# Optimization experiments

Hardware: AMD Instinct MI355X
Metric: run time of the kernel (lower is better)

## Reference

```python
import jax, jax.numpy as jnp
import numpy as np

N = 100000   # n_nodes
E = 1600000  # n_edges
BN_EPS = 1e-5


def setup_inputs() -> dict:
    key = jax.random.key(0)
    ks = jax.random.split(key, 10)
    x = jax.random.normal(ks[0], (N, 20), dtype=jnp.float32)
    edge_index = jax.random.randint(ks[1], (2, E), 0, N, dtype=jnp.int64)
    dims = [(20, 64), (64, 48), (48, 32)]
    inp = {"x": x, "edge_index": edge_index}
    for i, (di, do) in enumerate(dims):
        inp[f"W{i+1}"] = jax.random.normal(ks[2 + i], (di, do), dtype=jnp.float32) / np.sqrt(di)
        inp[f"b{i+1}"] = jnp.zeros((do,), dtype=jnp.float32)
        inp[f"g{i+1}"] = jnp.ones((do,), dtype=jnp.float32)
        inp[f"beta{i+1}"] = jnp.zeros((do,), dtype=jnp.float32)
    return inp


def _gcn_norm(edge_index):
    # add self loops, compute symmetric normalization D^-1/2 (A+I) D^-1/2
    loop = jnp.arange(N, dtype=edge_index.dtype)
    src = jnp.concatenate([edge_index[0], loop])
    dst = jnp.concatenate([edge_index[1], loop])
    deg = jax.ops.segment_sum(jnp.ones_like(src, dtype=jnp.float32), dst, num_segments=N)
    dinv = jax.lax.rsqrt(deg)  # deg >= 1 thanks to self loops
    norm = dinv[src] * dinv[dst]  # [E+N]
    return src, dst, norm


def _gcn_layer(h, src, dst, norm, W, b):
    m = h @ W                                  # [N, out]
    agg = jax.ops.segment_sum(m[src] * norm[:, None], dst, num_segments=N)
    return agg + b


def _batchnorm(x, g, beta):
    mu = jnp.mean(x, axis=0)
    var = jnp.mean(jnp.square(x - mu), axis=0)  # biased, as torch BN training
    return (x - mu) * jax.lax.rsqrt(var + BN_EPS) * g + beta


def reference(x, edge_index, W1, b1, g1, beta1, W2, b2, g2, beta2, W3, b3, g3, beta3):
    src, dst, norm = _gcn_norm(edge_index)
    h = _gcn_layer(x, src, dst, norm, W1, b1)
    h = jax.nn.relu(_batchnorm(h, g1, beta1))   # dropout rate 0 -> identity
    h = _gcn_layer(h, src, dst, norm, W2, b2)
    h = jax.nn.relu(_batchnorm(h, g2, beta2))
    h = _gcn_layer(h, src, dst, norm, W3, b3)
    h = _batchnorm(h, g3, beta3)                # last activation is Identity
    return h
```

## Files before the change

kernel.cpp:

```cpp
#include <hip/hip_runtime.h>


#define NN 100000
#define NE 1600000
constexpr float BN_EPS_F = 1e-5f;

#define BSZ 128
#define NBKT ((NN + BSZ - 1) / BSZ)
#define EC 16384
#define NEB ((NE + EC - 1) / EC)
#define MTOT (NBKT * NEB)
#define CAP 4096


__device__ __forceinline__ unsigned f2bf(float f) {
  union { float f; unsigned u; } v; v.f = f;
  return (v.u + 0x7fffu + ((v.u >> 16) & 1u)) >> 16;
}
__device__ __forceinline__ unsigned pack_bf2(float f0, float f1) {
  return f2bf(f0) | (f2bf(f1) << 16);
}
__device__ __forceinline__ float bf_lo(unsigned u) {
  union { unsigned u; float f; } v; v.u = u << 16; return v.f;
}
__device__ __forceinline__ float bf_hi(unsigned u) {
  union { unsigned u; float f; } v; v.u = u & 0xffff0000u; return v.f;
}


__global__ void hist_pass(const int* __restrict__ dst, int* __restrict__ ph, int e) {
  __shared__ int h[NBKT];
  int tid = threadIdx.x;
  for (int i = tid; i < NBKT; i += 256) h[i] = 0;
  __syncthreads();
  int tbase = blockIdx.x * EC + tid * 64;
#pragma unroll 4
  for (int k = 0; k < 64; k += 4) {
    int i = tbase + k;
    if (i < e) {
      int4 d = *(const int4*)(dst + i);
      atomicAdd(&h[d.x >> 7], 1);
      atomicAdd(&h[d.y >> 7], 1);
      atomicAdd(&h[d.z >> 7], 1);
      atomicAdd(&h[d.w >> 7], 1);
    }
  }
  __syncthreads();
  for (int i = tid; i < NBKT; i += 256) ph[i * NEB + blockIdx.x] = h[i];
}

__global__ void scan_block_sums(const int* __restrict__ data, int* __restrict__ bsums, int n) {
  __shared__ int sd[256];
  int tid = threadIdx.x;
  int base = blockIdx.x * 1024;
  int s = 0;
#pragma unroll
  for (int j = 0; j < 4; j++) {
    int idx = base + tid * 4 + j;
    if (idx < n) s += data[idx];
  }
  sd[tid] = s;
  __syncthreads();
  for (int o = 128; o > 0; o >>= 1) {
    if (tid < o) sd[tid] += sd[tid + o];
    __syncthreads();
  }
  if (tid == 0) bsums[blockIdx.x] = sd[0];
}

__global__ void scan_bsums2(int* __restrict__ bsums, int nb) {
  __shared__ int sd[128];
  int tid = threadIdx.x;
  int v = (tid < nb) ? bsums[tid] : 0;
  sd[tid] = v;
  __syncthreads();
  for (int o = 1; o < 128; o <<= 1) {
    int t = (tid >= o) ? sd[tid - o] : 0;
    __syncthreads();
    sd[tid] += t;
    __syncthreads();
  }
  if (tid < nb) bsums[tid] = sd[tid] - v;
}

__global__ void scan_apply(int* __restrict__ data, const int* __restrict__ bsums, int n) {
  __shared__ int sd[256];
  int tid = threadIdx.x;
  int base = blockIdx.x * 1024;
  int c[4];
  int s = 0;
#pragma unroll
  for (int j = 0; j < 4; j++) {
    int idx = base + tid * 4 + j;
    c[j] = (idx < n) ? data[idx] : 0;
    s += c[j];
  }
  sd[tid] = s;
  __syncthreads();
  for (int o = 1; o < 256; o <<= 1) {
    int t = (tid >= o) ? sd[tid - o] : 0;
    __syncthreads();
    sd[tid] += t;
    __syncthreads();
  }
  int off = bsums[blockIdx.x] + sd[tid] - s;
#pragma unroll
  for (int j = 0; j < 4; j++) {
    int idx = base + tid * 4 + j;
    if (idx < n) {
      data[idx] = off;
      off += c[j];
    }
  }
}

__global__ void bin_pass(const int* __restrict__ src, const int* __restrict__ dst,
                         const int* __restrict__ ph, int* __restrict__ packed, int e) {
  __shared__ int cur[NBKT];
  int tid = threadIdx.x;
  for (int i = tid; i < NBKT; i += 256) cur[i] = ph[i * NEB + blockIdx.x];
  __syncthreads();
  int tbase = blockIdx.x * EC + tid * 64;
#pragma unroll 4
  for (int k = 0; k < 64; k += 4) {
    int i = tbase + k;
    if (i < e) {
      int4 s = *(const int4*)(src + i);
      int4 d = *(const int4*)(dst + i);
      int p0 = atomicAdd(&cur[d.x >> 7], 1);
      int p1 = atomicAdd(&cur[d.y >> 7], 1);
      int p2 = atomicAdd(&cur[d.z >> 7], 1);
      int p3 = atomicAdd(&cur[d.w >> 7], 1);
      packed[p0] = (s.x << 7) | (d.x & 127);
      packed[p1] = (s.y << 7) | (d.y & 127);
      packed[p2] = (s.z << 7) | (d.z & 127);
      packed[p3] = (s.w << 7) | (d.w & 127);
    }
  }
}

__global__ void bucket_finalize(const int* __restrict__ ph, const int* __restrict__ packed,
                                const float* __restrict__ x, int* __restrict__ rowptr,
                                float* __restrict__ dinv, int* __restrict__ csr_src,
                                unsigned* __restrict__ xb) {
  __shared__ int eidx[CAP];
  __shared__ int csr_l[CAP];
  __shared__ int ldeg[BSZ], lscan[BSZ], lcur[BSZ];
  __shared__ float ldinv[BSZ];
  int b = blockIdx.x, tid = threadIdx.x;
  int start = ph[b * NEB];
  int end = (b == NBKT - 1) ? NE : ph[(b + 1) * NEB];
  int cnt = end - start;
  if (cnt > CAP) cnt = CAP;
  for (int i = tid; i < cnt; i += 256) eidx[i] = packed[start + i];
  if (tid < BSZ) ldeg[tid] = 0;
  __syncthreads();
  for (int i = tid; i < cnt; i += 256) atomicAdd(&ldeg[eidx[i] & 127], 1);
  __syncthreads();
  if (tid < BSZ) lscan[tid] = ldeg[tid];
  __syncthreads();
  for (int o = 1; o < BSZ; o <<= 1) {
    int t = 0;
    if (tid < BSZ && tid >= o) t = lscan[tid - o];
    __syncthreads();
    if (tid < BSZ) lscan[tid] += t;
    __syncthreads();
  }
  int gn = b * BSZ + tid;
  if (tid < BSZ) {
    int ex = lscan[tid] - ldeg[tid];
    lcur[tid] = ex;
    float dv = rsqrtf((float)(ldeg[tid] + 1));
    ldinv[tid] = dv;
    if (gn < NN) {
      rowptr[gn] = start + ex;
      dinv[gn] = dv;
    }
  }
  if (b == NBKT - 1 && tid == 0) rowptr[NN] = NE;
  __syncthreads();
  for (int i = tid; i < cnt; i += 256) {
    int pe = eidx[i];
    int pos = atomicAdd(&lcur[pe & 127], 1);
    csr_l[pos] = pe >> 7;
  }
  __syncthreads();
  for (int i = tid; i < cnt; i += 256) csr_src[start + i] = csr_l[i];
  for (int i = tid; i < BSZ * 16; i += 256) {
    int nl = i >> 4, j = i & 15;
    int g2 = b * BSZ + nl;
    if (g2 < NN) {
      unsigned u = 0;
      if (j < 10) {
        float2 f = *(const float2*)(x + (size_t)g2 * 20 + 2 * j);
        float dd = ldinv[nl];
        u = pack_bf2(dd * f.x, dd * f.y);
      }
      xb[(size_t)g2 * 16 + j] = u;
    }
  }
}


__launch_bounds__(256)
__global__ void aggregate_x(const unsigned* __restrict__ mb, const int* __restrict__ rowptr,
                            const int* __restrict__ csr_src, const float* __restrict__ dinv,
                            unsigned* __restrict__ out) {
  int tid = threadIdx.x;
  int sub = tid >> 4, lane = tid & 15;
  int cl = (lane < 10) ? lane : lane - 10;
  int d = blockIdx.x * 16 + sub;
  int start = rowptr[d], end = rowptr[d + 1];
  unsigned su = mb[(size_t)d * 16 + cl];
  float acc0 = bf_lo(su), acc1 = bf_hi(su);
  int j = start;
  int aligned = (start + 3) & ~3;
  int pe = aligned < end ? aligned : end;
  for (; j < pe; j++) {
    unsigned u = mb[(size_t)csr_src[j] * 16 + cl];
    acc0 += bf_lo(u); acc1 += bf_hi(u);
  }
  for (; j + 16 <= end; j += 16) {
    int4 s0 = *(const int4*)(csr_src + j);
    int4 s1 = *(const int4*)(csr_src + j + 4);
    int4 s2 = *(const int4*)(csr_src + j + 8);
    int4 s3 = *(const int4*)(csr_src + j + 12);
    int idx[16] = {s0.x, s0.y, s0.z, s0.w, s1.x, s1.y, s1.z, s1.w,
                   s2.x, s2.y, s2.z, s2.w, s3.x, s3.y, s3.z, s3.w};
    unsigned u[16];
#pragma unroll
    for (int t = 0; t < 16; t++) u[t] = mb[(size_t)idx[t] * 16 + cl];
#pragma unroll
    for (int t = 0; t < 16; t++) { acc0 += bf_lo(u[t]); acc1 += bf_hi(u[t]); }
  }
  for (; j + 4 <= end; j += 4) {
    int4 s0 = *(const int4*)(csr_src + j);
    unsigned u0 = mb[(size_t)s0.x * 16 + cl], u1 = mb[(size_t)s0.y * 16 + cl];
    unsigned u2 = mb[(size_t)s0.z * 16 + cl], u3 = mb[(size_t)s0.w * 16 + cl];
    acc0 += bf_lo(u0) + bf_lo(u1) + bf_lo(u2) + bf_lo(u3);
    acc1 += bf_hi(u0) + bf_hi(u1) + bf_hi(u2) + bf_hi(u3);
  }
  for (; j < end; j++) {
    unsigned u = mb[(size_t)csr_src[j] * 16 + cl];
    acc0 += bf_lo(u); acc1 += bf_hi(u);
  }
  float dd = dinv[d];
  unsigned uo = (lane < 10) ? pack_bf2(dd * acc0, dd * acc1) : 0u;
  out[(size_t)d * 16 + lane] = uo;
}


__launch_bounds__(256)
__global__ void aggregate_bf48(const uint2* __restrict__ mb, const int* __restrict__ rowptr,
                               const int* __restrict__ csr_src, const float* __restrict__ dinv,
                               const float* __restrict__ bias, unsigned* __restrict__ out,
                               float* __restrict__ gsum) {
  __shared__ float4 ssum[256], ssq[256];
  int tid = threadIdx.x;
  int sub = tid >> 4, lane = tid & 15;
  int cl = (lane < 12) ? lane : lane - 12;
  int d = blockIdx.x * 16 + sub;
  int start = rowptr[d], end = rowptr[d + 1];
  uint2 su = mb[(size_t)d * 12 + cl];
  float acc0 = bf_lo(su.x), acc1 = bf_hi(su.x), acc2 = bf_lo(su.y), acc3 = bf_hi(su.y);
  int j = start;
  int aligned = (start + 3) & ~3;
  int pe = aligned < end ? aligned : end;
  for (; j < pe; j++) {
    uint2 u = mb[(size_t)csr_src[j] * 12 + cl];
    acc0 += bf_lo(u.x); acc1 += bf_hi(u.x); acc2 += bf_lo(u.y); acc3 += bf_hi(u.y);
  }
  for (; j + 16 <= end; j += 16) {
    int4 s0 = *(const int4*)(csr_src + j);
    int4 s1 = *(const int4*)(csr_src + j + 4);
    int4 s2 = *(const int4*)(csr_src + j + 8);
    int4 s3 = *(const int4*)(csr_src + j + 12);
    int idx[16] = {s0.x, s0.y, s0.z, s0.w, s1.x, s1.y, s1.z, s1.w,
                   s2.x, s2.y, s2.z, s2.w, s3.x, s3.y, s3.z, s3.w};
    uint2 u[16];
#pragma unroll
    for (int t = 0; t < 16; t++) u[t] = mb[(size_t)idx[t] * 12 + cl];
#pragma unroll
    for (int t = 0; t < 16; t++) {
      acc0 += bf_lo(u[t].x); acc1 += bf_hi(u[t].x);
      acc2 += bf_lo(u[t].y); acc3 += bf_hi(u[t].y);
    }
  }
  for (; j + 4 <= end; j += 4) {
    int4 s0 = *(const int4*)(csr_src + j);
    uint2 u0 = mb[(size_t)s0.x * 12 + cl], u1 = mb[(size_t)s0.y * 12 + cl];
    uint2 u2 = mb[(size_t)s0.z * 12 + cl], u3 = mb[(size_t)s0.w * 12 + cl];
    acc0 += bf_lo(u0.x) + bf_lo(u1.x) + bf_lo(u2.x) + bf_lo(u3.x);
    acc1 += bf_hi(u0.x) + bf_hi(u1.x) + bf_hi(u2.x) + bf_hi(u3.x);
    acc2 += bf_lo(u0.y) + bf_lo(u1.y) + bf_lo(u2.y) + bf_lo(u3.y);
    acc3 += bf_hi(u0.y) + bf_hi(u1.y) + bf_hi(u2.y) + bf_hi(u3.y);
  }
  for (; j < end; j++) {
    uint2 u = mb[(size_t)csr_src[j] * 12 + cl];
    acc0 += bf_lo(u.x); acc1 += bf_hi(u.x); acc2 += bf_lo(u.y); acc3 += bf_hi(u.y);
  }
  float dd = dinv[d];
  float v0 = dd * acc0 + bias[4 * cl];
  float v1 = dd * acc1 + bias[4 * cl + 1];
  float v2 = dd * acc2 + bias[4 * cl + 2];
  float v3 = dd * acc3 + bias[4 * cl + 3];
  if (lane >= 12) { v0 = v1 = v2 = v3 = 0.f; }
  if (lane < 12) {
    uint2 uo = make_uint2(pack_bf2(v0, v1), pack_bf2(v2, v3));
    *(uint2*)(out + (size_t)d * 24 + 2 * cl) = uo;
  }
  ssum[tid] = make_float4(v0, v1, v2, v3);
  ssq[tid] = make_float4(v0 * v0, v1 * v1, v2 * v2, v3 * v3);
  __syncthreads();
  if (tid < 12) {
    float s0 = 0.f, s1 = 0.f, s2 = 0.f, s3 = 0.f;
    float q0 = 0.f, q1 = 0.f, q2 = 0.f, q3 = 0.f;
#pragma unroll
    for (int k = 0; k < 16; k++) {
      float4 a = ssum[k * 16 + tid];
      float4 b = ssq[k * 16 + tid];
      s0 += a.x; s1 += a.y; s2 += a.z; s3 += a.w;
      q0 += b.x; q1 += b.y; q2 += b.z; q3 += b.w;
    }
    float* gs = gsum + (blockIdx.x & 31) * 128;
    atomicAdd(&gs[4 * tid], s0);
    atomicAdd(&gs[4 * tid + 1], s1);
    atomicAdd(&gs[4 * tid + 2], s2);
    atomicAdd(&gs[4 * tid + 3], s3);
    atomicAdd(&gs[64 + 4 * tid], q0);
    atomicAdd(&gs[64 + 4 * tid + 1], q1);
    atomicAdd(&gs[64 + 4 * tid + 2], q2);
    atomicAdd(&gs[64 + 4 * tid + 3], q3);
  }
}


__launch_bounds__(256)
__global__ void aggregate_bf32(const unsigned* __restrict__ mb, const int* __restrict__ rowptr,
                               const int* __restrict__ csr_src, const float* __restrict__ dinv,
                               const float* __restrict__ bias, float* __restrict__ out,
                               float* __restrict__ gsum) {
  __shared__ float2 ssum[256], ssq[256];
  int tid = threadIdx.x;
  int sub = tid >> 4, lane = tid & 15;
  int d = blockIdx.x * 16 + sub;
  int start = rowptr[d], end = rowptr[d + 1];
  unsigned su = mb[(size_t)d * 16 + lane];
  float acc0 = bf_lo(su), acc1 = bf_hi(su);
  int j = start;
  int aligned = (start + 3) & ~3;
  int pe = aligned < end ? aligned : end;
  for (; j < pe; j++) {
    unsigned u = mb[(size_t)csr_src[j] * 16 + lane];
    acc0 += bf_lo(u); acc1 += bf_hi(u);
  }
  for (; j + 16 <= end; j += 16) {
    int4 s0 = *(const int4*)(csr_src + j);
    int4 s1 = *(const int4*)(csr_src + j + 4);
    int4 s2 = *(const int4*)(csr_src + j + 8);
    int4 s3 = *(const int4*)(csr_src + j + 12);
    int idx[16] = {s0.x, s0.y, s0.z, s0.w, s1.x, s1.y, s1.z, s1.w,
                   s2.x, s2.y, s2.z, s2.w, s3.x, s3.y, s3.z, s3.w};
    unsigned u[16];
#pragma unroll
    for (int t = 0; t < 16; t++) u[t] = mb[(size_t)idx[t] * 16 + lane];
#pragma unroll
    for (int t = 0; t < 16; t++) { acc0 += bf_lo(u[t]); acc1 += bf_hi(u[t]); }
  }
  for (; j + 4 <= end; j += 4) {
    int4 s0 = *(const int4*)(csr_src + j);
    unsigned u0 = mb[(size_t)s0.x * 16 + lane], u1 = mb[(size_t)s0.y * 16 + lane];
    unsigned u2 = mb[(size_t)s0.z * 16 + lane], u3 = mb[(size_t)s0.w * 16 + lane];
    acc0 += bf_lo(u0) + bf_lo(u1) + bf_lo(u2) + bf_lo(u3);
    acc1 += bf_hi(u0) + bf_hi(u1) + bf_hi(u2) + bf_hi(u3);
  }
  for (; j < end; j++) {
    unsigned u = mb[(size_t)csr_src[j] * 16 + lane];
    acc0 += bf_lo(u); acc1 += bf_hi(u);
  }
  float dd = dinv[d];
  float v0 = dd * acc0 + bias[2 * lane];
  float v1 = dd * acc1 + bias[2 * lane + 1];
  *(float2*)(out + (size_t)d * 32 + 2 * lane) = make_float2(v0, v1);
  ssum[tid] = make_float2(v0, v1);
  ssq[tid] = make_float2(v0 * v0, v1 * v1);
  __syncthreads();
  if (tid < 16) {
    float s0 = 0.f, s1 = 0.f, q0 = 0.f, q1 = 0.f;
#pragma unroll
    for (int k = 0; k < 16; k++) {
      float2 a = ssum[k * 16 + tid];
      float2 b = ssq[k * 16 + tid];
      s0 += a.x; s1 += a.y; q0 += b.x; q1 += b.y;
    }
    float* gs = gsum + (blockIdx.x & 31) * 128;
    atomicAdd(&gs[2 * tid], s0);
    atomicAdd(&gs[2 * tid + 1], s1);
    atomicAdd(&gs[64 + 2 * tid], q0);
    atomicAdd(&gs[64 + 2 * tid + 1], q1);
  }
}


__launch_bounds__(256)
__global__ void gemm1_stats(const unsigned* __restrict__ hu, const float* __restrict__ W,
                            const float* __restrict__ bias, unsigned* __restrict__ out,
                            float* __restrict__ gsum) {
  __shared__ float Wl[20 * 64];
  __shared__ float Hl[8][20];
  __shared__ float2 ssum[256], ssq[256];
  int tid = threadIdx.x;
  int row0 = blockIdx.x * 8;
  for (int i = tid; i < 20 * 64; i += 256) Wl[i] = W[i];
  if (tid < 128) {
    int r = tid >> 4, j = tid & 15;
    if (j < 10) {
      unsigned u = hu[(size_t)(row0 + r) * 16 + j];
      Hl[r][2 * j] = bf_lo(u);
      Hl[r][2 * j + 1] = bf_hi(u);
    }
  }
  __syncthreads();
  int r = tid >> 5, c2 = tid & 31;
  float acc0 = bias[2 * c2], acc1 = bias[2 * c2 + 1];
#pragma unroll
  for (int k = 0; k < 20; k++) {
    float a = Hl[r][k];
    acc0 = fmaf(a, Wl[k * 64 + 2 * c2], acc0);
    acc1 = fmaf(a, Wl[k * 64 + 2 * c2 + 1], acc1);
  }
  out[(size_t)(row0 + r) * 32 + c2] = pack_bf2(acc0, acc1);
  ssum[tid] = make_float2(acc0, acc1);
  ssq[tid] = make_float2(acc0 * acc0, acc1 * acc1);
  __syncthreads();
  if (tid < 32) {
    float s0 = 0.f, s1 = 0.f, q0 = 0.f, q1 = 0.f;
#pragma unroll
    for (int k = 0; k < 8; k++) {
      float2 a = ssum[k * 32 + tid];
      float2 b = ssq[k * 32 + tid];
      s0 += a.x; s1 += a.y; q0 += b.x; q1 += b.y;
    }
    float* gs = gsum + (blockIdx.x & 31) * 128;
    atomicAdd(&gs[2 * tid], s0);
    atomicAdd(&gs[2 * tid + 1], s1);
    atomicAdd(&gs[64 + 2 * tid], q0);
    atomicAdd(&gs[64 + 2 * tid + 1], q1);
  }
}


__launch_bounds__(256)
__global__ void gemm2_bf(const unsigned* __restrict__ hu, const float* __restrict__ W,
                         const float* __restrict__ scale, const float* __restrict__ shift,
                         const float* __restrict__ dinv, unsigned* __restrict__ out) {
  __shared__ float Wl[64 * 48];
  __shared__ float Hl[16][64];
  int tid = threadIdx.x;
  int row0 = blockIdx.x * 16;
  for (int i = tid; i < 64 * 48; i += 256) Wl[i] = W[i];
  for (int i = tid; i < 16 * 32; i += 256) {
    int r = i >> 5, j = i & 31;
    unsigned u = hu[(size_t)(row0 + r) * 32 + j];
    Hl[r][2 * j] = fmaxf(fmaf(bf_lo(u), scale[2 * j], shift[2 * j]), 0.f);
    Hl[r][2 * j + 1] = fmaxf(fmaf(bf_hi(u), scale[2 * j + 1], shift[2 * j + 1]), 0.f);
  }
  __syncthreads();
  int r = tid >> 4, c = tid & 15;
  if (c < 12) {
    float a0 = 0.f, a1 = 0.f, a2 = 0.f, a3 = 0.f;
#pragma unroll
    for (int k = 0; k < 64; k++) {
      float a = Hl[r][k];
      const float* w = &Wl[k * 48 + 4 * c];
      a0 = fmaf(a, w[0], a0);
      a1 = fmaf(a, w[1], a1);
      a2 = fmaf(a, w[2], a2);
      a3 = fmaf(a, w[3], a3);
    }
    float dd = dinv[row0 + r];
    uint2 uo = make_uint2(pack_bf2(dd * a0, dd * a1), pack_bf2(dd * a2, dd * a3));
    *(uint2*)(out + (size_t)(row0 + r) * 24 + 2 * c) = uo;
  }
}


__launch_bounds__(256)
__global__ void gemm3_bf(const unsigned* __restrict__ hu, const float* __restrict__ W,
                         const float* __restrict__ scale, const float* __restrict__ shift,
                         const float* __restrict__ dinv, unsigned* __restrict__ out) {
  __shared__ float Wl[48 * 32];
  __shared__ float Hl[16][48];
  int tid = threadIdx.x;
  int row0 = blockIdx.x * 16;
  for (int i = tid; i < 48 * 32; i += 256) Wl[i] = W[i];
  for (int i = tid; i < 16 * 24; i += 256) {
    int r = i / 24, j = i % 24;
    unsigned u = hu[(size_t)(row0 + r) * 24 + j];
    Hl[r][2 * j] = fmaxf(fmaf(bf_lo(u), scale[2 * j], shift[2 * j]), 0.f);
    Hl[r][2 * j + 1] = fmaxf(fmaf(bf_hi(u), scale[2 * j + 1], shift[2 * j + 1]), 0.f);
  }
  __syncthreads();
  int r = tid >> 4, c2 = tid & 15;
  float a0 = 0.f, a1 = 0.f;
#pragma unroll
  for (int k = 0; k < 48; k++) {
    float a = Hl[r][k];
    a0 = fmaf(a, Wl[k * 32 + 2 * c2], a0);
    a1 = fmaf(a, Wl[k * 32 + 2 * c2 + 1], a1);
  }
  float dd = dinv[row0 + r];
  out[(size_t)(row0 + r) * 16 + c2] = pack_bf2(dd * a0, dd * a1);
}


__global__ void bn_finalize(const float* __restrict__ gsum, const float* __restrict__ g,
                            const float* __restrict__ beta, float* __restrict__ scale,
                            float* __restrict__ shift, int C, float invn) {
  int i = threadIdx.x;
  if (i < C) {
    float s = 0.f, q = 0.f;
    for (int b = 0; b < 32; b++) {
      s += gsum[b * 128 + i];
      q += gsum[b * 128 + 64 + i];
    }
    float mean = s * invn;
    float var = q * invn - mean * mean;
    var = fmaxf(var, 0.f);
    float inv = rsqrtf(var + BN_EPS_F);
    float sc = g[i] * inv;
    scale[i] = sc;
    shift[i] = beta[i] - mean * sc;
  }
}

__global__ void bn_apply_out(const float* __restrict__ h, const float* __restrict__ scale,
                             const float* __restrict__ shift, float* __restrict__ out, int total) {
  int i = blockIdx.x * blockDim.x + threadIdx.x;
  if (i < total) {
    int c = i & 31;
    out[i] = h[i] * scale[c] + shift[c];
  }
}


extern "C" void kernel_launch(void* const* d_in, const int* in_sizes, int n_in,
                              void* d_out, int out_size, void* d_ws, size_t ws_size,
                              hipStream_t stream) {
  const float* x = (const float*)d_in[0];
  const int* ei = (const int*)d_in[1];
  const float* W1 = (const float*)d_in[2];
  const float* b1 = (const float*)d_in[3];
  const float* g1 = (const float*)d_in[4];
  const float* be1 = (const float*)d_in[5];
  const float* W2 = (const float*)d_in[6];
  const float* b2 = (const float*)d_in[7];
  const float* g2 = (const float*)d_in[8];
  const float* be2 = (const float*)d_in[9];
  const float* W3 = (const float*)d_in[10];
  const float* b3 = (const float*)d_in[11];
  const float* g3 = (const float*)d_in[12];
  const float* be3 = (const float*)d_in[13];
  float* out = (float*)d_out;

  const int* src = ei;
  const int* dst = ei + NE;

  char* ws = (char*)d_ws;
  size_t off = 0;
  auto alloc = [&](size_t bytes) -> void* {
    void* p = ws + off;
    off += bytes;
    off = (off + 255) & ~(size_t)255;
    return p;
  };
  int* ph = (int*)alloc((size_t)MTOT * 4);
  int* bsums = (int*)alloc(128 * 4);
  int* packed = (int*)alloc((size_t)NE * 4);
  int* rowptr = (int*)alloc((NN + 1) * 4);
  int* csr_src = (int*)alloc((size_t)NE * 4);
  float* dinv = (float*)alloc(NN * 4);
  float* gsum = (float*)alloc(3 * 32 * 128 * 4);
  float* scsh = (float*)alloc(3 * 128 * 4);
  unsigned* xb = (unsigned*)alloc((size_t)NN * 16 * 4);
  unsigned* aggx = (unsigned*)alloc((size_t)NN * 16 * 4);
  unsigned* h1u = (unsigned*)alloc((size_t)NN * 32 * 4);
  unsigned* m2b = (unsigned*)alloc((size_t)NN * 24 * 4);
  unsigned* h2u = (unsigned*)alloc((size_t)NN * 24 * 4);

  unsigned* m3b = aggx;
  float* h3 = (float*)h1u;

  hipMemsetAsync(gsum, 0, 3 * 32 * 128 * 4, stream);

  const int nscan = (MTOT + 1023) / 1024;
  hist_pass<<<NEB, 256, 0, stream>>>(dst, ph, NE);
  scan_block_sums<<<nscan, 256, 0, stream>>>(ph, bsums, MTOT);
  scan_bsums2<<<1, 128, 0, stream>>>(bsums, nscan);
  scan_apply<<<nscan, 256, 0, stream>>>(ph, bsums, MTOT);
  bin_pass<<<NEB, 256, 0, stream>>>(src, dst, ph, packed, NE);
  bucket_finalize<<<NBKT, 256, 0, stream>>>(ph, packed, x, rowptr, dinv, csr_src, xb);

  const float invn = 1.f / (float)NN;

  aggregate_x<<<NN / 16, 256, 0, stream>>>(xb, rowptr, csr_src, dinv, aggx);
  gemm1_stats<<<NN / 8, 256, 0, stream>>>(aggx, W1, b1, h1u, gsum);
  bn_finalize<<<1, 64, 0, stream>>>(gsum, g1, be1, scsh + 0, scsh + 64, 64, invn);

  gemm2_bf<<<NN / 16, 256, 0, stream>>>(h1u, W2, scsh + 0, scsh + 64, dinv, m2b);
  aggregate_bf48<<<NN / 16, 256, 0, stream>>>((const uint2*)m2b, rowptr, csr_src, dinv, b2, h2u,
                                              gsum + 4096);
  bn_finalize<<<1, 64, 0, stream>>>(gsum + 4096, g2, be2, scsh + 128, scsh + 192, 48, invn);

  gemm3_bf<<<NN / 16, 256, 0, stream>>>(h2u, W3, scsh + 128, scsh + 192, dinv, m3b);
  aggregate_bf32<<<NN / 16, 256, 0, stream>>>(m3b, rowptr, csr_src, dinv, b3, h3, gsum + 8192);
  bn_finalize<<<1, 64, 0, stream>>>(gsum + 8192, g3, be3, scsh + 256, scsh + 320, 32, invn);

  bn_apply_out<<<(NN * 32 + 255) / 256, 256, 0, stream>>>(h3, scsh + 256, scsh + 320, out, NN * 32);
}
```

Before: 340.9 us.

## Fuse layer-1 aggregation with GEMM1 and fold BN finalize into consumers

Merges the first aggregation with the layer-1 GEMM and its BN statistics in one kernel, so the aggregated-x intermediate is never written to or read back from global memory. The separate bn_finalize launches are removed; every block of gemm2, gemm3 and the output kernel now recomputes scale and shift from the partial sums itself. The layer-3 output is stored as bf16 instead of fp32, and the final BN apply is vectorized to four elements per thread. The cost is redundant per-block finalize work and a bf16 rounding step added to the last layer's output.

```diff
diff --git a/kernel.cpp b/kernel.cpp
--- a/kernel.cpp
+++ b/kernel.cpp
@@ -4,6 +4,7 @@
 #define NN 100000
 #define NE 1600000
 constexpr float BN_EPS_F = 1e-5f;
+constexpr float INVN = 1.f / (float)NN;
 
 #define BSZ 128
 #define NBKT ((NN + BSZ - 1) / BSZ)
@@ -203,10 +204,15 @@
 
 
 __launch_bounds__(256)
-__global__ void aggregate_x(const unsigned* __restrict__ mb, const int* __restrict__ rowptr,
-                            const int* __restrict__ csr_src, const float* __restrict__ dinv,
-                            unsigned* __restrict__ out) {
-  int tid = threadIdx.x;
+__global__ void agg1_gemm1(const unsigned* __restrict__ mb, const int* __restrict__ rowptr,
+                           const int* __restrict__ csr_src, const float* __restrict__ dinv,
+                           const float* __restrict__ W1, const float* __restrict__ b1,
+                           unsigned* __restrict__ h1u, float* __restrict__ gsum) {
+  __shared__ float Wl[20 * 64];
+  __shared__ float Hl[16][20];
+  __shared__ float4 sbuf[256];
+  int tid = threadIdx.x;
+  for (int i = tid; i < 20 * 64; i += 256) Wl[i] = W1[i];
   int sub = tid >> 4, lane = tid & 15;
   int cl = (lane < 10) ? lane : lane - 10;
   int d = blockIdx.x * 16 + sub;
@@ -245,8 +251,104 @@
     acc0 += bf_lo(u); acc1 += bf_hi(u);
   }
   float dd = dinv[d];
-  unsigned uo = (lane < 10) ? pack_bf2(dd * acc0, dd * acc1) : 0u;
-  out[(size_t)d * 16 + lane] = uo;
+  if (lane < 10) {
+    Hl[sub][2 * cl] = dd * acc0;
+    Hl[sub][2 * cl + 1] = dd * acc1;
+  }
+  __syncthreads();
+  int cg = lane;
+  float a0 = b1[4 * cg], a1 = b1[4 * cg + 1], a2 = b1[4 * cg + 2], a3 = b1[4 * cg + 3];
+#pragma unroll
+  for (int k = 0; k < 20; k++) {
+    float a = Hl[sub][k];
+    const float* w = &Wl[k * 64 + 4 * cg];
+    a0 = fmaf(a, w[0], a0);
+    a1 = fmaf(a, w[1], a1);
+    a2 = fmaf(a, w[2], a2);
+    a3 = fmaf(a, w[3], a3);
+  }
+  *(uint2*)(h1u + (size_t)d * 32 + 2 * cg) = make_uint2(pack_bf2(a0, a1), pack_bf2(a2, a3));
+  sbuf[tid] = make_float4(a0, a1, a2, a3);
+  __syncthreads();
+  float* gs = gsum + (blockIdx.x & 31) * 128;
+  if (tid < 16) {
+    float s0 = 0.f, s1 = 0.f, s2 = 0.f, s3 = 0.f;
+#pragma unroll
+    for (int k = 0; k < 16; k++) {
+      float4 a = sbuf[k * 16 + tid];
+      s0 += a.x; s1 += a.y; s2 += a.z; s3 += a.w;
+    }
+    atomicAdd(&gs[4 * tid], s0);
+    atomicAdd(&gs[4 * tid + 1], s1);
+    atomicAdd(&gs[4 * tid + 2], s2);
+    atomicAdd(&gs[4 * tid + 3], s3);
+  }
+  __syncthreads();
+  sbuf[tid] = make_float4(a0 * a0, a1 * a1, a2 * a2, a3 * a3);
+  __syncthreads();
+  if (tid < 16) {
+    float q0 = 0.f, q1 = 0.f, q2 = 0.f, q3 = 0.f;
+#pragma unroll
+    for (int k = 0; k < 16; k++) {
+      float4 b = sbuf[k * 16 + tid];
+      q0 += b.x; q1 += b.y; q2 += b.z; q3 += b.w;
+    }
+    atomicAdd(&gs[64 + 4 * tid], q0);
+    atomicAdd(&gs[64 + 4 * tid + 1], q1);
+    atomicAdd(&gs[64 + 4 * tid + 2], q2);
+    atomicAdd(&gs[64 + 4 * tid + 3], q3);
+  }
+}
+
+
+__launch_bounds__(256)
+__global__ void gemm2_bf(const unsigned* __restrict__ hu, const float* __restrict__ W,
+                         const float* __restrict__ gsum, const float* __restrict__ g,
+                         const float* __restrict__ beta, const float* __restrict__ dinv,
+                         unsigned* __restrict__ out) {
+  __shared__ float Wl[64 * 48];
+  __shared__ float Hl[16][64];
+  __shared__ float scl[64], sft[64];
+  int tid = threadIdx.x;
+  int row0 = blockIdx.x * 16;
+  if (tid < 64) {
+    float s = 0.f, q = 0.f;
+    for (int b = 0; b < 32; b++) {
+      s += gsum[b * 128 + tid];
+      q += gsum[b * 128 + 64 + tid];
+    }
+    float mean = s * INVN;
+    float var = fmaxf(q * INVN - mean * mean, 0.f);
+    float inv = rsqrtf(var + BN_EPS_F);
+    float sc = g[tid] * inv;
+    scl[tid] = sc;
+    sft[tid] = beta[tid] - mean * sc;
+  }
+  for (int i = tid; i < 64 * 48; i += 256) Wl[i] = W[i];
+  __syncthreads();
+  for (int i = tid; i < 16 * 32; i += 256) {
+    int r = i >> 5, j = i & 31;
+    unsigned u = hu[(size_t)(row0 + r) * 32 + j];
+    Hl[r][2 * j] = fmaxf(fmaf(bf_lo(u), scl[2 * j], sft[2 * j]), 0.f);
+    Hl[r][2 * j + 1] = fmaxf(fmaf(bf_hi(u), scl[2 * j + 1], sft[2 * j + 1]), 0.f);
+  }
+  __syncthreads();
+  int r = tid >> 4, c = tid & 15;
+  if (c < 12) {
+    float a0 = 0.f, a1 = 0.f, a2 = 0.f, a3 = 0.f;
+#pragma unroll
+    for (int k = 0; k < 64; k++) {
+      float a = Hl[r][k];
+      const float* w = &Wl[k * 48 + 4 * c];
+      a0 = fmaf(a, w[0], a0);
+      a1 = fmaf(a, w[1], a1);
+      a2 = fmaf(a, w[2], a2);
+      a3 = fmaf(a, w[3], a3);
+    }
+    float dd = dinv[row0 + r];
+    uint2 uo = make_uint2(pack_bf2(dd * a0, dd * a1), pack_bf2(dd * a2, dd * a3));
+    *(uint2*)(out + (size_t)(row0 + r) * 24 + 2 * c) = uo;
+  }
 }
 
 
@@ -255,7 +357,7 @@
                                const int* __restrict__ csr_src, const float* __restrict__ dinv,
                                const float* __restrict__ bias, unsigned* __restrict__ out,
                                float* __restrict__ gsum) {
-  __shared__ float4 ssum[256], ssq[256];
+  __shared__ float4 sbuf[256];
   int tid = threadIdx.x;
   int sub = tid >> 4, lane = tid & 15;
   int cl = (lane < 12) ? lane : lane - 12;
@@ -309,24 +411,31 @@
     uint2 uo = make_uint2(pack_bf2(v0, v1), pack_bf2(v2, v3));
     *(uint2*)(out + (size_t)d * 24 + 2 * cl) = uo;
   }
-  ssum[tid] = make_float4(v0, v1, v2, v3);
-  ssq[tid] = make_float4(v0 * v0, v1 * v1, v2 * v2, v3 * v3);
-  __syncthreads();
+  sbuf[tid] = make_float4(v0, v1, v2, v3);
+  __syncthreads();
+  float* gs = gsum + (blockIdx.x & 31) * 128;
   if (tid < 12) {
     float s0 = 0.f, s1 = 0.f, s2 = 0.f, s3 = 0.f;
-    float q0 = 0.f, q1 = 0.f, q2 = 0.f, q3 = 0.f;
 #pragma unroll
     for (int k = 0; k < 16; k++) {
-      float4 a = ssum[k * 16 + tid];
-      float4 b = ssq[k * 16 + tid];
+      float4 a = sbuf[k * 16 + tid];
       s0 += a.x; s1 += a.y; s2 += a.z; s3 += a.w;
-      q0 += b.x; q1 += b.y; q2 += b.z; q3 += b.w;
-    }
-    float* gs = gsum + (blockIdx.x & 31) * 128;
+    }
     atomicAdd(&gs[4 * tid], s0);
     atomicAdd(&gs[4 * tid + 1], s1);
     atomicAdd(&gs[4 * tid + 2], s2);
     atomicAdd(&gs[4 * tid + 3], s3);
+  }
+  __syncthreads();
+  sbuf[tid] = make_float4(v0 * v0, v1 * v1, v2 * v2, v3 * v3);
+  __syncthreads();
+  if (tid < 12) {
+    float q0 = 0.f, q1 = 0.f, q2 = 0.f, q3 = 0.f;
+#pragma unroll
+    for (int k = 0; k < 16; k++) {
+      float4 b = sbuf[k * 16 + tid];
+      q0 += b.x; q1 += b.y; q2 += b.z; q3 += b.w;
+    }
     atomicAdd(&gs[64 + 4 * tid], q0);
     atomicAdd(&gs[64 + 4 * tid + 1], q1);
     atomicAdd(&gs[64 + 4 * tid + 2], q2);
@@ -336,9 +445,54 @@
 
 
 __launch_bounds__(256)
+__global__ void gemm3_bf(const unsigned* __restrict__ hu, const float* __restrict__ W,
+                         const float* __restrict__ gsum, const float* __restrict__ g,
+                         const float* __restrict__ beta, const float* __restrict__ dinv,
+                         unsigned* __restrict__ out) {
+  __shared__ float Wl[48 * 32];
+  __shared__ float Hl[16][48];
+  __shared__ float scl[48], sft[48];
+  int tid = threadIdx.x;
+  int row0 = blockIdx.x * 16;
+  if (tid < 48) {
+    float s = 0.f, q = 0.f;
+    for (int b = 0; b < 32; b++) {
+      s += gsum[b * 128 + tid];
+      q += gsum[b * 128 + 64 + tid];
+    }
+    float mean = s * INVN;
+    float var = fmaxf(q * INVN - mean * mean, 0.f);
+    float inv = rsqrtf(var + BN_EPS_F);
+    float sc = g[tid] * inv;
+    scl[tid] = sc;
+    sft[tid] = beta[tid] - mean * sc;
+  }
+  for (int i = tid; i < 48 * 32; i += 256) Wl[i] = W[i];
+  __syncthreads();
+  for (int i = tid; i < 16 * 24; i += 256) {
+    int r = i / 24, j = i % 24;
+    unsigned u = hu[(size_t)(row0 + r) * 24 + j];
+    Hl[r][2 * j] = fmaxf(fmaf(bf_lo(u), scl[2 * j], sft[2 * j]), 0.f);
+    Hl[r][2 * j + 1] = fmaxf(fmaf(bf_hi(u), scl[2 * j + 1], sft[2 * j + 1]), 0.f);
+  }
+  __syncthreads();
+  int r = tid >> 4, c2 = tid & 15;
+  float a0 = 0.f, a1 = 0.f;
+#pragma unroll
+  for (int k = 0; k < 48; k++) {
+    float a = Hl[r][k];
+    a0 = fmaf(a, Wl[k * 32 + 2 * c2], a0);
+    a1 = fmaf(a, Wl[k * 32 + 2 * c2 + 1], a1);
+  }
+  float dd = dinv[row0 + r];
+  out[(size_t)(row0 + r) * 16 + c2] = pack_bf2(dd * a0, dd * a1);
+}
+
+
+__launch_bounds__(256)
 __global__ void aggregate_bf32(const unsigned* __restrict__ mb, const int* __restrict__ rowptr,
                                const int* __restrict__ csr_src, const float* __restrict__ dinv,
-                               const float* __restrict__ bias, float* __restrict__ out,
+                               const float* __restrict__ bias, unsigned* __restrict__ out,
                                float* __restrict__ gsum) {
   __shared__ float2 ssum[256], ssq[256];
   int tid = threadIdx.x;
@@ -381,7 +535,7 @@
   float dd = dinv[d];
   float v0 = dd * acc0 + bias[2 * lane];
   float v1 = dd * acc1 + bias[2 * lane + 1];
-  *(float2*)(out + (size_t)d * 32 + 2 * lane) = make_float2(v0, v1);
+  out[(size_t)d * 16 + lane] = pack_bf2(v0, v1);
   ssum[tid] = make_float2(v0, v1);
   ssq[tid] = make_float2(v0 * v0, v1 * v1);
   __syncthreads();
@@ -403,144 +557,35 @@
 
 
 __launch_bounds__(256)
-__global__ void gemm1_stats(const unsigned* __restrict__ hu, const float* __restrict__ W,
-                            const float* __restrict__ bias, unsigned* __restrict__ out,
-                            float* __restrict__ gsum) {
-  __shared__ float Wl[20 * 64];
-  __shared__ float Hl[8][20];
-  __shared__ float2 ssum[256], ssq[256];
-  int tid = threadIdx.x;
-  int row0 = blockIdx.x * 8;
-  for (int i = tid; i < 20 * 64; i += 256) Wl[i] = W[i];
-  if (tid < 128) {
-    int r = tid >> 4, j = tid & 15;
-    if (j < 10) {
-      unsigned u = hu[(size_t)(row0 + r) * 16 + j];
-      Hl[r][2 * j] = bf_lo(u);
-      Hl[r][2 * j + 1] = bf_hi(u);
-    }
-  }
-  __syncthreads();
-  int r = tid >> 5, c2 = tid & 31;
-  float acc0 = bias[2 * c2], acc1 = bias[2 * c2 + 1];
-#pragma unroll
-  for (int k = 0; k < 20; k++) {
-    float a = Hl[r][k];
-    acc0 = fmaf(a, Wl[k * 64 + 2 * c2], acc0);
-    acc1 = fmaf(a, Wl[k * 64 + 2 * c2 + 1], acc1);
-  }
-  out[(size_t)(row0 + r) * 32 + c2] = pack_bf2(acc0, acc1);
-  ssum[tid] = make_float2(acc0, acc1);
-  ssq[tid] = make_float2(acc0 * acc0, acc1 * acc1);
-  __syncthreads();
+__global__ void bn_apply_out(const unsigned* __restrict__ hu, const float* __restrict__ gsum,
+                             const float* __restrict__ g, const float* __restrict__ beta,
+                             float* __restrict__ out) {
+  __shared__ float scl[32], sft[32];
+  int tid = threadIdx.x;
   if (tid < 32) {
-    float s0 = 0.f, s1 = 0.f, q0 = 0.f, q1 = 0.f;
-#pragma unroll
-    for (int k = 0; k < 8; k++) {
-      float2 a = ssum[k * 32 + tid];
-      float2 b = ssq[k * 32 + tid];
-      s0 += a.x; s1 += a.y; q0 += b.x; q1 += b.y;
-    }
-    float* gs = gsum + (blockIdx.x & 31) * 128;
-    atomicAdd(&gs[2 * tid], s0);
-    atomicAdd(&gs[2 * tid + 1], s1);
-    atomicAdd(&gs[64 + 2 * tid], q0);
-    atomicAdd(&gs[64 + 2 * tid + 1], q1);
-  }
-}
-
-
-__launch_bounds__(256)
-__global__ void gemm2_bf(const unsigned* __restrict__ hu, const float* __restrict__ W,
-                         const float* __restrict__ scale, const float* __restrict__ shift,
-                         const float* __restrict__ dinv, unsigned* __restrict__ out) {
-  __shared__ float Wl[64 * 48];
-  __shared__ float Hl[16][64];
-  int tid = threadIdx.x;
-  int row0 = blockIdx.x * 16;
-  for (int i = tid; i < 64 * 48; i += 256) Wl[i] = W[i];
-  for (int i = tid; i < 16 * 32; i += 256) {
-    int r = i >> 5, j = i & 31;
-    unsigned u = hu[(size_t)(row0 + r) * 32 + j];
-    Hl[r][2 * j] = fmaxf(fmaf(bf_lo(u), scale[2 * j], shift[2 * j]), 0.f);
-    Hl[r][2 * j + 1] = fmaxf(fmaf(bf_hi(u), scale[2 * j + 1], shift[2 * j + 1]), 0.f);
-  }
-  __syncthreads();
-  int r = tid >> 4, c = tid & 15;
-  if (c < 12) {
-    float a0 = 0.f, a1 = 0.f, a2 = 0.f, a3 = 0.f;
-#pragma unroll
-    for (int k = 0; k < 64; k++) {
-      float a = Hl[r][k];
-      const float* w = &Wl[k * 48 + 4 * c];
-      a0 = fmaf(a, w[0], a0);
-      a1 = fmaf(a, w[1], a1);
-      a2 = fmaf(a, w[2], a2);
-      a3 = fmaf(a, w[3], a3);
-    }
-    float dd = dinv[row0 + r];
-    uint2 uo = make_uint2(pack_bf2(dd * a0, dd * a1), pack_bf2(dd * a2, dd * a3));
-    *(uint2*)(out + (size_t)(row0 + r) * 24 + 2 * c) = uo;
-  }
-}
-
-
-__launch_bounds__(256)
-__global__ void gemm3_bf(const unsigned* __restrict__ hu, const float* __restrict__ W,
-                         const float* __restrict__ scale, const float* __restrict__ shift,
-                         const float* __restrict__ dinv, unsigned* __restrict__ out) {
-  __shared__ float Wl[48 * 32];
-  __shared__ float Hl[16][48];
-  int tid = threadIdx.x;
-  int row0 = blockIdx.x * 16;
-  for (int i = tid; i < 48 * 32; i += 256) Wl[i] = W[i];
-  for (int i = tid; i < 16 * 24; i += 256) {
-    int r = i / 24, j = i % 24;
-    unsigned u = hu[(size_t)(row0 + r) * 24 + j];
-    Hl[r][2 * j] = fmaxf(fmaf(bf_lo(u), scale[2 * j], shift[2 * j]), 0.f);
-    Hl[r][2 * j + 1] = fmaxf(fmaf(bf_hi(u), scale[2 * j + 1], shift[2 * j + 1]), 0.f);
-  }
-  __syncthreads();
-  int r = tid >> 4, c2 = tid & 15;
-  float a0 = 0.f, a1 = 0.f;
-#pragma unroll
-  for (int k = 0; k < 48; k++) {
-    float a = Hl[r][k];
-    a0 = fmaf(a, Wl[k * 32 + 2 * c2], a0);
-    a1 = fmaf(a, Wl[k * 32 + 2 * c2 + 1], a1);
-  }
-  float dd = dinv[row0 + r];
-  out[(size_t)(row0 + r) * 16 + c2] = pack_bf2(dd * a0, dd * a1);
-}
-
-
-__global__ void bn_finalize(const float* __restrict__ gsum, const float* __restrict__ g,
-                            const float* __restrict__ beta, float* __restrict__ scale,
-                            float* __restrict__ shift, int C, float invn) {
-  int i = threadIdx.x;
-  if (i < C) {
     float s = 0.f, q = 0.f;
     for (int b = 0; b < 32; b++) {
-      s += gsum[b * 128 + i];
-      q += gsum[b * 128 + 64 + i];
-    }
-    float mean = s * invn;
-    float var = q * invn - mean * mean;
-    var = fmaxf(var, 0.f);
+      s += gsum[b * 128 + tid];
+      q += gsum[b * 128 + 64 + tid];
+    }
+    float mean = s * INVN;
+    float var = fmaxf(q * INVN - mean * mean, 0.f);
     float inv = rsqrtf(var + BN_EPS_F);
-    float sc = g[i] * inv;
-    scale[i] = sc;
-    shift[i] = beta[i] - mean * sc;
-  }
-}
-
-__global__ void bn_apply_out(const float* __restrict__ h, const float* __restrict__ scale,
-                             const float* __restrict__ shift, float* __restrict__ out, int total) {
-  int i = blockIdx.x * blockDim.x + threadIdx.x;
-  if (i < total) {
-    int c = i & 31;
-    out[i] = h[i] * scale[c] + shift[c];
-  }
+    float sc = g[tid] * inv;
+    scl[tid] = sc;
+    sft[tid] = beta[tid] - mean * sc;
+  }
+  __syncthreads();
+  int base = (blockIdx.x * 256 + tid) * 4;
+  int node = base >> 5;
+  int c0 = base & 31;
+  uint2 u = *(const uint2*)(hu + (size_t)node * 16 + (c0 >> 1));
+  float4 o;
+  o.x = bf_lo(u.x) * scl[c0] + sft[c0];
+  o.y = bf_hi(u.x) * scl[c0 + 1] + sft[c0 + 1];
+  o.z = bf_lo(u.y) * scl[c0 + 2] + sft[c0 + 2];
+  o.w = bf_hi(u.y) * scl[c0 + 3] + sft[c0 + 3];
+  *(float4*)(out + base) = o;
 }
 
 
@@ -581,15 +626,13 @@
   int* csr_src = (int*)alloc((size_t)NE * 4);
   float* dinv = (float*)alloc(NN * 4);
   float* gsum = (float*)alloc(3 * 32 * 128 * 4);
-  float* scsh = (float*)alloc(3 * 128 * 4);
   unsigned* xb = (unsigned*)alloc((size_t)NN * 16 * 4);
-  unsigned* aggx = (unsigned*)alloc((size_t)NN * 16 * 4);
   unsigned* h1u = (unsigned*)alloc((size_t)NN * 32 * 4);
   unsigned* m2b = (unsigned*)alloc((size_t)NN * 24 * 4);
   unsigned* h2u = (unsigned*)alloc((size_t)NN * 24 * 4);
 
-  unsigned* m3b = aggx;
-  float* h3 = (float*)h1u;
+  unsigned* m3b = xb;
+  unsigned* h3u = h1u;
 
   hipMemsetAsync(gsum, 0, 3 * 32 * 128 * 4, stream);
 
@@ -601,20 +644,14 @@
   bin_pass<<<NEB, 256, 0, stream>>>(src, dst, ph, packed, NE);
   bucket_finalize<<<NBKT, 256, 0, stream>>>(ph, packed, x, rowptr, dinv, csr_src, xb);
 
-  const float invn = 1.f / (float)NN;
-
-  aggregate_x<<<NN / 16, 256, 0, stream>>>(xb, rowptr, csr_src, dinv, aggx);
-  gemm1_stats<<<NN / 8, 256, 0, stream>>>(aggx, W1, b1, h1u, gsum);
-  bn_finalize<<<1, 64, 0, stream>>>(gsum, g1, be1, scsh + 0, scsh + 64, 64, invn);
-
-  gemm2_bf<<<NN / 16, 256, 0, stream>>>(h1u, W2, scsh + 0, scsh + 64, dinv, m2b);
+  agg1_gemm1<<<NN / 16, 256, 0, stream>>>(xb, rowptr, csr_src, dinv, W1, b1, h1u, gsum);
+
+  gemm2_bf<<<NN / 16, 256, 0, stream>>>(h1u, W2, gsum, g1, be1, dinv, m2b);
   aggregate_bf48<<<NN / 16, 256, 0, stream>>>((const uint2*)m2b, rowptr, csr_src, dinv, b2, h2u,
                                               gsum + 4096);
-  bn_finalize<<<1, 64, 0, stream>>>(gsum + 4096, g2, be2, scsh + 128, scsh + 192, 48, invn);
-
-  gemm3_bf<<<NN / 16, 256, 0, stream>>>(h2u, W3, scsh + 128, scsh + 192, dinv, m3b);
-  aggregate_bf32<<<NN / 16, 256, 0, stream>>>(m3b, rowptr, csr_src, dinv, b3, h3, gsum + 8192);
-  bn_finalize<<<1, 64, 0, stream>>>(gsum + 8192, g3, be3, scsh + 256, scsh + 320, 32, invn);
-
-  bn_apply_out<<<(NN * 32 + 255) / 256, 256, 0, stream>>>(h3, scsh + 256, scsh + 320, out, NN * 32);
-}
+
+  gemm3_bf<<<NN / 16, 256, 0, stream>>>(h2u, W3, gsum + 4096, g2, be2, dinv, m3b);
+  aggregate_bf32<<<NN / 16, 256, 0, stream>>>(m3b, rowptr, csr_src, dinv, b3, h3u, gsum + 8192);
+
+  bn_apply_out<<<NN * 32 / 1024, 256, 0, stream>>>(h3u, gsum + 8192, g3, be3, out);
+}
```

Result: no change. 335.0 us (-1.7%).
